# Performance work log

Hardware: AMD Instinct MI355X
Metric: run time of the kernel (lower is better)

Reference implementation:

```python
import jax, jax.numpy as jnp
import numpy as np

N = 4096  # layer_size
R = 4     # displacement rank
B = 8192  # batch
STD = 0.01

def setup_inputs() -> dict:
    key = jax.random.key(0)
    kx, kg, kh = jax.random.split(key, 3)
    x = jax.random.normal(kx, (B, N), dtype=jnp.float32)
    G = (jax.random.normal(kg, (N, R), dtype=jnp.float32) * STD)
    H = (jax.random.normal(kh, (N, R), dtype=jnp.float32) * STD)
    return {"x": x, "G": G, "H": H}

def _krylov(f_corner, V):
    """Stack of Z_f^k V for k = 0..N-1, where Z_f is the unit lower shift
    matrix with corner entry f (Z_mult_fn in the original code):
    (Z_f v)[0] = f * v[N-1], (Z_f v)[i] = v[i-1].
    Returns cols of shape (N, N, R) indexed [power, row, rank]."""
    n = V.shape[0]
    def step(v, _):
        v_next = jnp.concatenate([f_corner * v[-1:], v[:-1]], axis=0)
        return v_next, v
    _, cols = jax.lax.scan(step, V, None, length=n)
    return cols

def reference(x, G, H):
    # Stein displacement reconstruction for toeplitz_like:
    # W = 0.5 * sum_i Krylov(Z_1, g_i) @ Krylov(Z_{-1}, h_i)^T
    K_A = _krylov(jnp.float32(1.0), G)    # (N, N, R)
    K_B = _krylov(jnp.float32(-1.0), H)   # (N, N, R)
    W = 0.5 * jnp.einsum('knr,kmr->nm', K_A, K_B)  # (N, N)
    return x @ W
```

## Files before the change

### kernel.cpp

```cpp
#include <hip/hip_runtime.h>
#include <hip/hip_bf16.h>


constexpr int N = 4096;
constexpr int BATCH = 8192;
constexpr int BK = 32;
constexpr int NT = N / BK;

typedef _Float16 f16;
typedef __attribute__((ext_vector_type(8))) f16 half8;
typedef __attribute__((ext_vector_type(4))) float f32x4;

__global__ __launch_bounds__(256) void build_T_kernel(const float* __restrict__ G,
                                                      const float* __restrict__ H,
                                                      float* __restrict__ T) {
    const int d = blockIdx.x;
    const int tid = threadIdx.x;
    const int lane = tid & 63;
    const int wid = tid >> 6;
    const int j0 = tid * 16;

    float pref[16];
    float s = 0.f;
#pragma unroll
    for (int i = 0; i < 16; ++i) {
        const int j = j0 + i;
        const float4 g4 = *reinterpret_cast<const float4*>(G + (size_t)((d + j) & (N - 1)) * 4);
        const float4 h4 = *reinterpret_cast<const float4*>(H + (size_t)j * 4);
        s += g4.x * h4.x + g4.y * h4.y + g4.z * h4.z + g4.w * h4.w;
        pref[i] = s;
    }

    float v = s;
#pragma unroll
    for (int off = 1; off < 64; off <<= 1) {
        const float u = __shfl_up(v, off, 64);
        if (lane >= off) v += u;
    }
    __shared__ float wsum[4];
    if (lane == 63) wsum[wid] = v;
    __syncthreads();
    const float w0 = wsum[0], w1 = wsum[1], w2 = wsum[2], w3 = wsum[3];
    const float total = w0 + w1 + w2 + w3;
    float wpref = 0.f;
    if (wid > 0) wpref += w0;
    if (wid > 1) wpref += w1;
    if (wid > 2) wpref += w2;
    const float excl = wpref + (v - s);
    const float halfc = 0.5f * total;

    float* out = T + (size_t)d * N + j0;
#pragma unroll
    for (int i = 0; i < 16; ++i) out[i] = excl + pref[i] - halfc;
}

__global__ __launch_bounds__(256) void gather_Wt_f16_kernel(const float* __restrict__ T,
                                                            f16* __restrict__ Wt) {
    __shared__ float tile[128][67];
    const int n0 = blockIdx.x * 64;
    const int m0 = blockIdx.y * 64;
    const int d0 = (n0 - m0 - 63) & (N - 1);
    const int t = threadIdx.x;

#pragma unroll
    for (int i = 0; i < 32; ++i) {
        const int flat = t + i * 256;
        const int row = flat >> 6;
        const int col = flat & 63;
        tile[row][col] = T[(size_t)((d0 + row) & (N - 1)) * N + m0 + col];
    }
    __syncthreads();
#pragma unroll
    for (int i = 0; i < 2; ++i) {
        const int lm = (t >> 3) + i * 32;
        const int ln0 = (t & 7) * 8;
        half8 v;
#pragma unroll
        for (int e = 0; e < 8; ++e) v[e] = (f16)tile[ln0 + e - lm + 63][lm];
        *reinterpret_cast<half8*>(Wt + (size_t)(m0 + lm) * N + n0 + ln0) = v;
    }
}

__global__ __launch_bounds__(256) void gather_W_kernel(const float* __restrict__ T,
                                                       float* __restrict__ W) {
    __shared__ float tile[128][64];
    const int m0 = blockIdx.x * 64;
    const int n0 = blockIdx.y * 64;
    const int d0 = (n0 - m0 - 63) & (N - 1);
    const int t = threadIdx.x;

#pragma unroll
    for (int i = 0; i < 32; ++i) {
        const int flat = t + i * 256;
        const int row = flat >> 6;
        const int col = flat & 63;
        tile[row][col] = T[(size_t)((d0 + row) & (N - 1)) * N + m0 + col];
    }
    __syncthreads();
#pragma unroll
    for (int i = 0; i < 16; ++i) {
        const int flat = t + i * 256;
        const int ln = flat >> 6;
        const int lm = flat & 63;
        W[(size_t)(n0 + ln) * N + m0 + lm] = tile[ln - lm + 63][lm];
    }
}

__global__ __launch_bounds__(256) void cast_x_f16_kernel(const float* __restrict__ x,
                                                         f16* __restrict__ xh) {
    const long long total8 = (long long)BATCH * N / 8;
    for (long long i = (long long)blockIdx.x * 256 + threadIdx.x; i < total8;
         i += (long long)gridDim.x * 256) {
        const float4 a = reinterpret_cast<const float4*>(x)[2 * i];
        const float4 b = reinterpret_cast<const float4*>(x)[2 * i + 1];
        half8 v;
        v[0] = (f16)a.x; v[1] = (f16)a.y; v[2] = (f16)a.z; v[3] = (f16)a.w;
        v[4] = (f16)b.x; v[5] = (f16)b.y; v[6] = (f16)b.z; v[7] = (f16)b.w;
        *reinterpret_cast<half8*>(xh + i * 8) = v;
    }
}

__device__ inline void gll16(const void* g, void* l) {
    __builtin_amdgcn_global_load_lds(
        (const __attribute__((address_space(1))) void*)g,
        (__attribute__((address_space(3))) void*)l, 16, 0, 0);
}

__global__ __launch_bounds__(256) void gemm_f16_kernel(const f16* __restrict__ X,
                                                       const f16* __restrict__ Wt,
                                                       float* __restrict__ C) {
    __shared__ f16 As[2][4096];
    __shared__ f16 Bs[2][4096];

    const int bn0 = blockIdx.x * 128;
    const int bm0 = blockIdx.y * 128;
    const int t = threadIdx.x;
    const int lane = t & 63;
    const int w = t >> 6;
    const int wm = w >> 1, wn = w & 1;
    const int lr = lane & 15;
    const int lk = lane >> 4;
    const int chl = lk ^ ((lr >> 1) & 3);

    f32x4 acc[4][4];
    const f32x4 zero = {0.f, 0.f, 0.f, 0.f};
#pragma unroll
    for (int i = 0; i < 4; ++i)
#pragma unroll
        for (int j = 0; j < 4; ++j) acc[i][j] = zero;

    auto stage = [&](int kt, int buf) {
        const int k0 = kt * BK;
#pragma unroll
        for (int i = 0; i < 2; ++i) {
            const int f = t + i * 256;
            const int row = f >> 2;
            const int kc = (f & 3) ^ ((f >> 3) & 3);
            gll16(X  + (size_t)(bm0 + row) * N + k0 + kc * 8, (char*)&As[buf][0] + f * 16);
            gll16(Wt + (size_t)(bn0 + row) * N + k0 + kc * 8, (char*)&Bs[buf][0] + f * 16);
        }
    };
    auto compute = [&](int buf) {
        half8 a[4], b[4];
#pragma unroll
        for (int q = 0; q < 4; ++q) {
            const int ar = wm * 64 + q * 16 + lr;
            const int br = wn * 64 + q * 16 + lr;
            a[q] = *reinterpret_cast<const half8*>(&As[buf][(ar * 4 + chl) * 8]);
            b[q] = *reinterpret_cast<const half8*>(&Bs[buf][(br * 4 + chl) * 8]);
        }
        __builtin_amdgcn_s_setprio(1);
#pragma unroll
        for (int mf = 0; mf < 4; ++mf)
#pragma unroll
            for (int nf = 0; nf < 4; ++nf)
                acc[mf][nf] = __builtin_amdgcn_mfma_f32_16x16x32_f16(a[mf], b[nf], acc[mf][nf], 0, 0, 0);
        __builtin_amdgcn_s_setprio(0);
    };

    stage(0, 0);
    __syncthreads();
    for (int kt = 0; kt < NT; kt += 2) {
        stage(kt + 1, 1);
        compute(0);
        __syncthreads();
        if (kt + 2 < NT) stage(kt + 2, 0);
        compute(1);
        __syncthreads();
    }

#pragma unroll
    for (int mf = 0; mf < 4; ++mf)
#pragma unroll
        for (int nf = 0; nf < 4; ++nf)
#pragma unroll
            for (int r = 0; r < 4; ++r)
                C[(size_t)(bm0 + wm * 64 + mf * 16 + lk * 4 + r) * N +
                  bn0 + wn * 64 + nf * 16 + lr] = acc[mf][nf][r];
}

__global__ __launch_bounds__(256) void gemm_f32_kernel(const float* __restrict__ A,
                                                       const float* __restrict__ B,
                                                       float* __restrict__ C) {
    __shared__ float Asf[16][132];
    __shared__ float Bsf[16][128];

    const int t = threadIdx.x;
    const int bn0 = blockIdx.x * 128;
    const int bm0 = blockIdx.y * 128;
    const int tx = t & 15;
    const int ty = t >> 4;

    float acc[8][8] = {};

    for (int k0 = 0; k0 < N; k0 += 16) {
#pragma unroll
        for (int i = 0; i < 2; ++i) {
            const int flat4 = t + i * 256;
            const int r = flat4 >> 2;
            const int q = flat4 & 3;
            const float4 av =
                *reinterpret_cast<const float4*>(A + (size_t)(bm0 + r) * N + k0 + q * 4);
            Asf[q * 4 + 0][r] = av.x;
            Asf[q * 4 + 1][r] = av.y;
            Asf[q * 4 + 2][r] = av.z;
            Asf[q * 4 + 3][r] = av.w;
            const int rb = flat4 >> 5;
            const int qb = flat4 & 31;
            *reinterpret_cast<float4*>(&Bsf[rb][qb * 4]) =
                *reinterpret_cast<const float4*>(B + (size_t)(k0 + rb) * N + bn0 + qb * 4);
        }
        __syncthreads();
#pragma unroll
        for (int k = 0; k < 16; ++k) {
            float a[8], b[8];
            *reinterpret_cast<float4*>(a)     = *reinterpret_cast<const float4*>(&Asf[k][ty * 8]);
            *reinterpret_cast<float4*>(a + 4) = *reinterpret_cast<const float4*>(&Asf[k][ty * 8 + 4]);
            *reinterpret_cast<float4*>(b)     = *reinterpret_cast<const float4*>(&Bsf[k][tx * 8]);
            *reinterpret_cast<float4*>(b + 4) = *reinterpret_cast<const float4*>(&Bsf[k][tx * 8 + 4]);
#pragma unroll
            for (int e = 0; e < 8; ++e)
#pragma unroll
                for (int f = 0; f < 8; ++f) acc[e][f] += a[e] * b[f];
        }
        __syncthreads();
    }

#pragma unroll
    for (int e = 0; e < 8; ++e) {
        float* crow = C + (size_t)(bm0 + ty * 8 + e) * N + bn0 + tx * 8;
        *reinterpret_cast<float4*>(crow)     = *reinterpret_cast<const float4*>(&acc[0] + e * 8);
        *reinterpret_cast<float4*>(crow + 4) = *reinterpret_cast<const float4*>(&acc[0] + e * 8 + 4);
    }
}

extern "C" void kernel_launch(void* const* d_in, const int* in_sizes, int n_in,
                              void* d_out, int out_size, void* d_ws, size_t ws_size,
                              hipStream_t stream) {
    const float* x = (const float*)d_in[0];
    const float* G = (const float*)d_in[1];
    const float* H = (const float*)d_in[2];
    float* out = (float*)d_out;

    char* ws = (char*)d_ws;
    const size_t SZ_T  = (size_t)N * N * sizeof(float);
    const size_t SZ_Wt = (size_t)N * N * 2;
    const size_t SZ_X  = (size_t)BATCH * N * 2;

    float* T = nullptr;
    f16 *Wt = nullptr, *Xh = nullptr;
    bool f16_path = false;

    if (ws_size >= SZ_T + SZ_Wt + SZ_X) {
        T  = (float*)ws;
        Wt = (f16*)(ws + SZ_T);
        Xh = (f16*)(ws + SZ_T + SZ_Wt);
        f16_path = true;
    } else if (ws_size >= SZ_Wt + SZ_X) {
        T  = (float*)d_out;
        Wt = (f16*)ws;
        Xh = (f16*)(ws + SZ_Wt);
        f16_path = true;
    }

    if (f16_path) {
        build_T_kernel<<<dim3(N), dim3(256), 0, stream>>>(G, H, T);
        gather_Wt_f16_kernel<<<dim3(N / 64, N / 64), dim3(256), 0, stream>>>(T, Wt);
        cast_x_f16_kernel<<<dim3(2048), dim3(256), 0, stream>>>(x, Xh);
        gemm_f16_kernel<<<dim3(N / 128, BATCH / 128), dim3(256), 0, stream>>>(Xh, Wt, out);
    } else {
        float* Tf = (float*)d_out;
        float* W  = (float*)ws;
        build_T_kernel<<<dim3(N), dim3(256), 0, stream>>>(G, H, Tf);
        gather_W_kernel<<<dim3(N / 64, N / 64), dim3(256), 0, stream>>>(Tf, W);
        gemm_f32_kernel<<<dim3(N / 128, BATCH / 128), dim3(256), 0, stream>>>(x, W, out);
    }
}
```

Measured before the change: 729.0 us.

## Enlarge f16 GEMM tile to 256x256 with 512 threads and split-phase compute

```diff
diff --git a/kernel.cpp b/kernel.cpp
--- a/kernel.cpp
+++ b/kernel.cpp
@@ -126,26 +126,26 @@
         (__attribute__((address_space(3))) void*)l, 16, 0, 0);
 }
 
-__global__ __launch_bounds__(256) void gemm_f16_kernel(const f16* __restrict__ X,
+__global__ __launch_bounds__(512) void gemm_f16_kernel(const f16* __restrict__ X,
                                                        const f16* __restrict__ Wt,
                                                        float* __restrict__ C) {
-    __shared__ f16 As[2][4096];
-    __shared__ f16 Bs[2][4096];
-
-    const int bn0 = blockIdx.x * 128;
-    const int bm0 = blockIdx.y * 128;
+    __shared__ f16 As[2][8192];
+    __shared__ f16 Bs[2][8192];
+
+    const int bn0 = blockIdx.x * 256;
+    const int bm0 = blockIdx.y * 256;
     const int t = threadIdx.x;
     const int lane = t & 63;
     const int w = t >> 6;
-    const int wm = w >> 1, wn = w & 1;
+    const int wm = w >> 2;
+    const int wn = w & 3;
     const int lr = lane & 15;
     const int lk = lane >> 4;
-    const int chl = lk ^ ((lr >> 1) & 3);
-
-    f32x4 acc[4][4];
+
+    f32x4 acc[8][4];
     const f32x4 zero = {0.f, 0.f, 0.f, 0.f};
 #pragma unroll
-    for (int i = 0; i < 4; ++i)
+    for (int i = 0; i < 8; ++i)
 #pragma unroll
         for (int j = 0; j < 4; ++j) acc[i][j] = zero;
 
@@ -153,21 +153,31 @@
         const int k0 = kt * BK;
 #pragma unroll
         for (int i = 0; i < 2; ++i) {
-            const int f = t + i * 256;
+            const int f = t + i * 512;
             const int row = f >> 2;
-            const int kc = (f & 3) ^ ((f >> 3) & 3);
-            gll16(X  + (size_t)(bm0 + row) * N + k0 + kc * 8, (char*)&As[buf][0] + f * 16);
-            gll16(Wt + (size_t)(bn0 + row) * N + k0 + kc * 8, (char*)&Bs[buf][0] + f * 16);
+            const int ko = (f & 3) * 8;
+            gll16(X  + (size_t)(bm0 + row) * N + k0 + ko, (char*)&As[buf][0] + f * 16);
+            gll16(Wt + (size_t)(bn0 + row) * N + k0 + ko, (char*)&Bs[buf][0] + f * 16);
         }
     };
-    auto compute = [&](int buf) {
+
+    stage(0, 0);
+    __syncthreads();
+
+    for (int kt = 0; kt < NT; ++kt) {
+        const int buf = kt & 1;
+        if (kt + 1 < NT) stage(kt + 1, buf ^ 1);
+
         half8 a[4], b[4];
 #pragma unroll
         for (int q = 0; q < 4; ++q) {
-            const int ar = wm * 64 + q * 16 + lr;
             const int br = wn * 64 + q * 16 + lr;
-            a[q] = *reinterpret_cast<const half8*>(&As[buf][(ar * 4 + chl) * 8]);
-            b[q] = *reinterpret_cast<const half8*>(&Bs[buf][(br * 4 + chl) * 8]);
+            b[q] = *reinterpret_cast<const half8*>(&Bs[buf][br * 32 + lk * 8]);
+        }
+#pragma unroll
+        for (int q = 0; q < 4; ++q) {
+            const int ar = wm * 128 + q * 16 + lr;
+            a[q] = *reinterpret_cast<const half8*>(&As[buf][ar * 32 + lk * 8]);
         }
         __builtin_amdgcn_s_setprio(1);
 #pragma unroll
@@ -176,26 +186,32 @@
             for (int nf = 0; nf < 4; ++nf)
                 acc[mf][nf] = __builtin_amdgcn_mfma_f32_16x16x32_f16(a[mf], b[nf], acc[mf][nf], 0, 0, 0);
         __builtin_amdgcn_s_setprio(0);
-    };
-
-    stage(0, 0);
-    __syncthreads();
-    for (int kt = 0; kt < NT; kt += 2) {
-        stage(kt + 1, 1);
-        compute(0);
+
+        __builtin_amdgcn_s_barrier();
+
+#pragma unroll
+        for (int q = 0; q < 4; ++q) {
+            const int ar = wm * 128 + (q + 4) * 16 + lr;
+            a[q] = *reinterpret_cast<const half8*>(&As[buf][ar * 32 + lk * 8]);
+        }
+        __builtin_amdgcn_s_setprio(1);
+#pragma unroll
+        for (int mf = 0; mf < 4; ++mf)
+#pragma unroll
+            for (int nf = 0; nf < 4; ++nf)
+                acc[mf + 4][nf] = __builtin_amdgcn_mfma_f32_16x16x32_f16(a[mf], b[nf], acc[mf + 4][nf], 0, 0, 0);
+        __builtin_amdgcn_s_setprio(0);
+
         __syncthreads();
-        if (kt + 2 < NT) stage(kt + 2, 0);
-        compute(1);
-        __syncthreads();
-    }
-
-#pragma unroll
-    for (int mf = 0; mf < 4; ++mf)
+    }
+
+#pragma unroll
+    for (int mf = 0; mf < 8; ++mf)
 #pragma unroll
         for (int nf = 0; nf < 4; ++nf)
 #pragma unroll
             for (int r = 0; r < 4; ++r)
-                C[(size_t)(bm0 + wm * 64 + mf * 16 + lk * 4 + r) * N +
+                C[(size_t)(bm0 + wm * 128 + mf * 16 + lk * 4 + r) * N +
                   bn0 + wn * 64 + nf * 16 + lr] = acc[mf][nf][r];
 }
 
@@ -287,7 +303,7 @@
         build_T_kernel<<<dim3(N), dim3(256), 0, stream>>>(G, H, T);
         gather_Wt_f16_kernel<<<dim3(N / 64, N / 64), dim3(256), 0, stream>>>(T, Wt);
         cast_x_f16_kernel<<<dim3(2048), dim3(256), 0, stream>>>(x, Xh);
-        gemm_f16_kernel<<<dim3(N / 128, BATCH / 128), dim3(256), 0, stream>>>(Xh, Wt, out);
+        gemm_f16_kernel<<<dim3(N / 256, BATCH / 256), dim3(512), 0, stream>>>(Xh, Wt, out);
     } else {
         float* Tf = (float*)d_out;
         float* W  = (float*)ws;
```

After: 727.8 us. Within noise of the previous version (-0.2%).
